# Kernel tuning notes

Measured on AMD Instinct MI355X. Metric: run time of the kernel, lower is better.

## Reference

```python
import jax, jax.numpy as jnp
import numpy as np

ITER_STEPS = 2  # matches init_kwargs iteration_steps


def setup_inputs() -> dict:
    key = jax.random.key(0)
    ks = jax.random.split(key, 7)
    B, N, D = 16, 1024, 128
    s = 1.0 / np.sqrt(D).astype(np.float32)
    return {
        "node": jax.random.normal(ks[0], (B, N, D), jnp.float32),
        "node_mask": jax.random.randint(ks[1], (B, N), 0, 2, jnp.int32),
        "graph": jax.random.randint(ks[2], (B, N, N), 0, 2, jnp.int32),
        "w_weight": jax.random.normal(ks[3], (D, 1), jnp.float32) * s,
        "b_weight": jnp.zeros((1,), jnp.float32),
        "w_self": jax.random.normal(ks[4], (D, D), jnp.float32) * s,
        "b_self": jnp.zeros((D,), jnp.float32),
        "w_left": jax.random.normal(ks[5], (D, D), jnp.float32) * s,
        "w_right": jax.random.normal(ks[6], (D, D), jnp.float32) * s,
    }


def reference(node, node_mask, graph, w_weight, b_weight, w_self, b_self, w_left, w_right):
    B, N, D = node.shape
    dt = node.dtype
    nm = node_mask.astype(dt)
    g = graph.astype(dt)  # graph[:, :N, :N] slice is identity here
    diag = jnp.eye(N, dtype=dt)
    # pairwise validity mask, zero diagonal (no self loops)
    pair = nm[:, None, :] * nm[:, :, None] * (1.0 - diag)
    gl = pair * g            # edges present in graph
    gr = pair * (1.0 - g)    # complement edges
    nnum = gl.sum(-1) + gr.sum(-1)
    # replace_masked_values(nnum, nnum>=1, 1): avoid div-by-zero for isolated nodes
    nnum = jnp.where(nnum >= 1.0, nnum, jnp.ones((), dt))
    ws = []
    for _ in range(ITER_STEPS):
        node_weight = jax.nn.sigmoid(node @ w_weight + b_weight)[..., 0]  # [B, N]
        ws.append(node_weight)
        self_info = node @ w_self + b_self
        # replace_masked_values(weight_bcast, mask, 0) == weight * mask (mask is 0/1)
        left = jnp.einsum('bij,bjd->bid', node_weight[:, None, :] * gl, node @ w_left)
        right = jnp.einsum('bij,bjd->bid', node_weight[:, None, :] * gr, node @ w_right)
        node = jax.nn.relu(self_info + (left + right) / nnum[..., None])
    all_node_weight = jnp.stack(ws, axis=1)  # [B, ITER_STEPS, N]
    return node, all_node_weight
```

## Files before the change

### kernel.cpp

```cpp
#include <hip/hip_runtime.h>
#include <math.h>


constexpr int B = 16, N = 1024, D = 128, ITERS = 2;

typedef unsigned short u16;
typedef unsigned char u8;
typedef unsigned int u32;
typedef __attribute__((ext_vector_type(8))) short short8v;
typedef __attribute__((ext_vector_type(4))) unsigned int uint4v;
typedef __attribute__((ext_vector_type(4))) float float4v;

__device__ inline u16 f32_to_bf16(float f) {
  u32 bits = __float_as_uint(f);
  bits += 0x7FFFu + ((bits >> 16) & 1u);
  return (u16)(bits >> 16);
}

__device__ __forceinline__ short8v expand_byte(u32 by) {
  u32 e0 = ((by & 1u) ? 0x3F80u : 0u) | ((by & 2u) ? 0x3F800000u : 0u);
  u32 e1 = ((by & 4u) ? 0x3F80u : 0u) | ((by & 8u) ? 0x3F800000u : 0u);
  u32 e2 = ((by & 16u) ? 0x3F80u : 0u) | ((by & 32u) ? 0x3F800000u : 0u);
  u32 e3 = ((by & 64u) ? 0x3F80u : 0u) | ((by & 128u) ? 0x3F800000u : 0u);
  uint4v ev = {e0, e1, e2, e3};
  return __builtin_bit_cast(short8v, ev);
}

__device__ __forceinline__ void map_brt(int blk, int& b, int& rt) {
  int slot = blk >> 3;
  b = ((slot >> 6) << 3) | (blk & 7);
  rt = slot & 63;
}

__global__ __launch_bounds__(256) void wpack_kernel(
    const float* __restrict__ w_self, const float* __restrict__ w_left,
    const float* __restrict__ w_right, const int* __restrict__ mask,
    u16* __restrict__ wsF, u16* __restrict__ wlF, u16* __restrict__ wrF,
    float* __restrict__ sb) {
  int blk = blockIdx.x, tid = threadIdx.x;
  if (blk < 12) {
    int widx = blk >> 2, seg = blk & 3;
    const float* W = (widx == 0) ? w_self : (widx == 1) ? w_left : w_right;
    u16* WF = (widx == 0) ? wsF : (widx == 1) ? wlF : wrF;
#pragma unroll
    for (int q = 0; q < 16; ++q) {
      int o = seg * 4096 + q * 256 + tid;
      int e = o & 7, lane = (o >> 3) & 63, ks = (o >> 9) & 3, cblk = o >> 11;
      int c = cblk * 16 + (lane & 15);
      int k = ks * 32 + ((lane >> 4) & 3) * 8 + e;
      WF[o] = f32_to_bf16(W[k * 128 + c]);
    }
  } else {
    int b = tid >> 4, seg = tid & 15;
    const int* mp = mask + b * N + seg * 64;
    int s = 0;
    for (int q = 0; q < 64; ++q) s += mp[q];
    float fs = (float)s;
    fs += __shfl_xor(fs, 8, 16);
    fs += __shfl_xor(fs, 4, 16);
    fs += __shfl_xor(fs, 2, 16);
    fs += __shfl_xor(fs, 1, 16);
    if (seg == 0) sb[b] = fs;
  }
}

__device__ __forceinline__ void prep_body(
    float (*nlds)[132], float* wmrow, float* invrow, int b, int rt, int tid,
    const int* __restrict__ mask, const float* __restrict__ w_weight,
    const float* __restrict__ b_weight, const float* __restrict__ b_self,
    const u16* __restrict__ wsF, const u16* __restrict__ wlF,
    const u16* __restrict__ wrF, const float* __restrict__ sb,
    float* __restrict__ outw_t, float* __restrict__ nsadj, u16* __restrict__ xF,
    float* __restrict__ part) {
  int r0 = rt * 16;
  if (tid < 128) {
    int r = tid >> 3, jj = tid & 7;
    float acc = 0.f;
#pragma unroll
    for (int q = 0; q < 4; ++q) {
      float4 wv = *(const float4*)(w_weight + jj * 16 + q * 4);
      const float* np = &nlds[r][jj * 16 + q * 4];
      acc += np[0] * wv.x + np[1] * wv.y + np[2] * wv.z + np[3] * wv.w;
    }
    acc += __shfl_xor(acc, 4, 8);
    acc += __shfl_xor(acc, 2, 8);
    acc += __shfl_xor(acc, 1, 8);
    if (jj == 0) {
      float w = 1.f / (1.f + expf(-(acc + b_weight[0])));
      outw_t[b * (ITERS * N) + r0 + r] = w;
      float nm = (float)mask[b * N + r0 + r];
      float nnum = fmaxf(nm * (sb[b] - nm), 1.f);
      wmrow[r] = w * nm;
      invrow[r] = nm / nnum;
    }
  }
  __syncthreads();

  int w = tid >> 6, lane = tid & 63;
  int l15 = lane & 15, lg = lane >> 4;
  int ch = w * 32;

  short8v af[4];
#pragma unroll
  for (int ks = 0; ks < 4; ++ks) {
    float tmp[8];
    *(float4*)&tmp[0] = *(const float4*)&nlds[l15][ks * 32 + lg * 8];
    *(float4*)&tmp[4] = *(const float4*)&nlds[l15][ks * 32 + lg * 8 + 4];
    short8v t;
#pragma unroll
    for (int e = 0; e < 8; ++e) t[e] = (short)f32_to_bf16(tmp[e]);
    af[ks] = t;
  }

  float4v aNR[2], aNL[2], aNS[2];
#define RUN_GEMM(WF, ACC)                                                          \
  {                                                                                \
    _Pragma("unroll") for (int cf = 0; cf < 2; ++cf) {                             \
      ACC[cf] = (float4v){0.f, 0.f, 0.f, 0.f};                                     \
      int cblk = w * 2 + cf;                                                       \
      const u16* bp = (WF) + (((cblk * 4) * 64 + lane) << 3);                      \
      _Pragma("unroll") for (int ks = 0; ks < 4; ++ks) {                           \
        short8v bf = *(const short8v*)(bp + ks * 512);                             \
        ACC[cf] =                                                                  \
            __builtin_amdgcn_mfma_f32_16x16x32_bf16(af[ks], bf, ACC[cf], 0, 0, 0); \
      }                                                                            \
    }                                                                              \
  }
  RUN_GEMM(wrF, aNR);
  RUN_GEMM(wlF, aNL);
  RUN_GEMM(wsF, aNS);
#undef RUN_GEMM

  float wmv[4], invv[4];
#pragma unroll
  for (int j = 0; j < 4; ++j) {
    int rloc = lg * 4 + j;
    wmv[j] = wmrow[rloc];
    invv[j] = invrow[rloc];
  }
  int kch = rt >> 1;
  int lane_f = ((rt & 1) * 2 + (lg >> 1)) * 16;
  int e0 = (lg & 1) * 4;
  float pv[2] = {0.f, 0.f};
#pragma unroll
  for (int cf = 0; cf < 2; ++cf) {
    int col = ch + cf * 16 + l15;
    float bsv = b_self[col];
    u16 xb[4];
#pragma unroll
    for (int j = 0; j < 4; ++j) {
      float x = wmv[j] * (aNL[cf][j] - aNR[cf][j]);
      float v = wmv[j] * aNR[cf][j];
      pv[cf] += v;
      nsadj[((size_t)b * N + r0 + lg * 4 + j) * D + col] =
          aNS[cf][j] + bsv - invv[j] * v;
      xb[j] = f32_to_bf16(x);
    }
    int cblk = w * 2 + cf;
    size_t fi = ((((size_t)b * 8 + cblk) * 32 + kch) * 64 + lane_f + l15) * 8 + e0;
    *(ushort4*)&xF[fi] = *(ushort4*)&xb[0];
  }
#pragma unroll
  for (int cf = 0; cf < 2; ++cf) {
    pv[cf] += __shfl_xor(pv[cf], 16);
    pv[cf] += __shfl_xor(pv[cf], 32);
  }
  if (lg == 0) {
#pragma unroll
    for (int cf = 0; cf < 2; ++cf)
      part[((size_t)b * 64 + rt) * 128 + ch + cf * 16 + l15] = pv[cf];
  }
}

__device__ __forceinline__ void agg32_core(
    const u8* __restrict__ gpk, const u16* __restrict__ xF,
    const float* __restrict__ part, const float* __restrict__ sb,
    const int* __restrict__ mask, const float* __restrict__ nsadj, int b, int r0,
    int tid, float (*red)[128], float ov[8]) {
  {
    int col = tid & 127, grp = tid >> 7;
    float s = 0.f;
#pragma unroll
    for (int p = 0; p < 16; ++p)
      s += part[((size_t)b * 64 + grp * 16 + p) * 128 + col];
    red[grp][col] = s;
  }
  int wv = tid >> 6, lane = tid & 63;
  int l15 = lane & 15, lg = lane >> 4;

  const u8* g0 = gpk + ((size_t)b * N + r0 + l15) * 128 + lg * 32;
  uint4 qA = *(const uint4*)g0;
  uint4 qB = *(const uint4*)(g0 + 16);
  uint4 qC = *(const uint4*)(g0 + 16 * 128);
  uint4 qD = *(const uint4*)(g0 + 16 * 128 + 16);
  u32 q0[8] = {qA.x, qA.y, qA.z, qA.w, qB.x, qB.y, qB.z, qB.w};
  u32 q1[8] = {qC.x, qC.y, qC.z, qC.w, qD.x, qD.y, qD.z, qD.w};

  const u16* xb = xF + (((size_t)b * 8 + wv) * 32) * 512 + lane * 8;

  float4v acc0 = {0.f, 0.f, 0.f, 0.f};
  float4v acc1 = {0.f, 0.f, 0.f, 0.f};
  short8v b0 = *(const short8v*)(xb);
  short8v b1 = *(const short8v*)(xb + 512);
#pragma unroll
  for (int cl = 0; cl < 32; ++cl) {
    short8v b2 = b0;
    if (cl + 2 < 32) b2 = *(const short8v*)(xb + (cl + 2) * 512);
    u32 by0 = (q0[cl >> 2] >> ((cl & 3) * 8)) & 255u;
    u32 by1 = (q1[cl >> 2] >> ((cl & 3) * 8)) & 255u;
    short8v a0 = expand_byte(by0);
    short8v a1 = expand_byte(by1);
    acc0 = __builtin_amdgcn_mfma_f32_16x16x32_bf16(a0, b0, acc0, 0, 0, 0);
    acc1 = __builtin_amdgcn_mfma_f32_16x16x32_bf16(a1, b0, acc1, 0, 0, 0);
    b0 = b1;
    b1 = b2;
  }
  __syncthreads();

  float sbv = sb[b];
  int col = wv * 16 + l15;
  float vt = red[0][col] + red[1][col] + red[2][col] + red[3][col];
#pragma unroll
  for (int rs = 0; rs < 2; ++rs) {
#pragma unroll
    for (int j = 0; j < 4; ++j) {
      float a = (rs == 0) ? acc0[j] : acc1[j];
      int orow = r0 + rs * 16 + lg * 4 + j;
      float nm = (float)mask[b * N + orow];
      float nnum = fmaxf(nm * (sbv - nm), 1.f);
      float inv = nm / nnum;
      size_t off = ((size_t)b * N + orow) * D + col;
      ov[rs * 4 + j] = fmaxf(nsadj[off] + inv * (a + vt), 0.f);
    }
  }
}

__device__ __forceinline__ void map_brt32(int blk, int& b, int& rt32) {
  int slot = blk >> 3;
  b = ((slot >> 5) << 3) | (blk & 7);
  rt32 = slot & 31;
}

__global__ __launch_bounds__(256, 4) void pack_prep_kernel(
    const float* __restrict__ node, const int* __restrict__ graph,
    const int* __restrict__ mask, const float* __restrict__ w_weight,
    const float* __restrict__ b_weight, const float* __restrict__ b_self,
    const u16* __restrict__ wsF, const u16* __restrict__ wlF,
    const u16* __restrict__ wrF, const float* __restrict__ sb,
    u8* __restrict__ gpk, float* __restrict__ outw, float* __restrict__ nsadjA,
    u16* __restrict__ xFA, float* __restrict__ partA) {
  __shared__ float nlds[16][132];
  __shared__ float wmrow[16], invrow[16];
  int tid = threadIdx.x;
  int blk = blockIdx.x;

  if (blk < 2048) {
    int gidx0 = blk * 256 + tid;
    int4 ra[4][2];
#pragma unroll
    for (int it = 0; it < 4; ++it) {
      int gidx = gidx0 + it * (2048 * 256);
      int j = gidx & 127, rowg = gidx >> 7;
      const int* gp = graph + ((size_t)rowg << 10) + j * 8;
      ra[it][0] = *(const int4*)gp;
      ra[it][1] = *(const int4*)(gp + 4);
    }
#pragma unroll
    for (int it = 0; it < 4; ++it) {
      int gidx = gidx0 + it * (2048 * 256);
      int j = gidx & 127, rowg = gidx >> 7;
      int i = rowg & (N - 1);
      int4 a = ra[it][0], c = ra[it][1];
      u32 by = (u32)(a.x != 0) | ((u32)(a.y != 0) << 1) | ((u32)(a.z != 0) << 2) |
               ((u32)(a.w != 0) << 3) | ((u32)(c.x != 0) << 4) |
               ((u32)(c.y != 0) << 5) | ((u32)(c.z != 0) << 6) |
               ((u32)(c.w != 0) << 7);
      if (j == (i >> 3)) by &= ~(1u << (i & 7));
      gpk[((size_t)rowg << 7) + (j & 3) * 32 + (j >> 2)] = (u8)by;
    }
    return;
  }

  int pblk = blk - 2048;
  int b, rt;
  map_brt(pblk, b, rt);
  int r0 = rt * 16;

  const float* nbase = node + ((size_t)b * N + r0) * D;
#pragma unroll
  for (int p = 0; p < 2; ++p) {
    int g = p * 256 + tid;
    int row = g >> 5, c4 = g & 31;
    *(float4*)&nlds[row][c4 * 4] = *(const float4*)(nbase + row * 128 + c4 * 4);
  }
  __syncthreads();

  prep_body(nlds, wmrow, invrow, b, rt, tid, mask, w_weight, b_weight, b_self, wsF,
            wlF, wrF, sb, outw, nsadjA, xFA, partA);
}

__global__ __launch_bounds__(512, 4) void agg_prep_kernel(
    const u8* __restrict__ gpk, const int* __restrict__ mask,
    const float* __restrict__ w_weight, const float* __restrict__ b_weight,
    const float* __restrict__ b_self, const u16* __restrict__ wsF,
    const u16* __restrict__ wlF, const u16* __restrict__ wrF,
    const float* __restrict__ sb, const float* __restrict__ nsadjA,
    const u16* __restrict__ xFA, const float* __restrict__ partA,
    float* __restrict__ outw, float* __restrict__ nsadjB, u16* __restrict__ xFB,
    float* __restrict__ partB) {
  __shared__ float red[4][128];
  __shared__ float nlds[32][132];
  __shared__ float wmrow[32], invrow[32];
  int tid = threadIdx.x;
  int b, rt32;
  map_brt32(blockIdx.x, b, rt32);
  int r0 = rt32 * 32;

  float ov[8];
  agg32_core(gpk, xFA, partA, sb, mask, nsadjA, b, r0, tid, red, ov);

  int wv = tid >> 6, lane = tid & 63;
  int l15 = lane & 15, lg = lane >> 4;
  int col = wv * 16 + l15;
#pragma unroll
  for (int rs = 0; rs < 2; ++rs)
#pragma unroll
    for (int j = 0; j < 4; ++j) nlds[rs * 16 + lg * 4 + j][col] = ov[rs * 4 + j];
  __syncthreads();

  int half = tid >> 8;
  int tid2 = tid & 255;
  prep_body((float(*)[132]) & nlds[half * 16][0], &wmrow[half * 16],
            &invrow[half * 16], b, rt32 * 2 + half, tid2, mask, w_weight,
            b_weight, b_self, wsF, wlF, wrF, sb, outw + N, nsadjB, xFB, partB);
}

__global__ __launch_bounds__(512, 4) void agg_fin_kernel(
    const u8* __restrict__ gpk, const int* __restrict__ mask,
    const float* __restrict__ sb, const float* __restrict__ nsadjB,
    const u16* __restrict__ xFB, const float* __restrict__ partB,
    float* __restrict__ out) {
  __shared__ float red[4][128];
  int tid = threadIdx.x;
  int b, rt32;
  map_brt32(blockIdx.x, b, rt32);
  int r0 = rt32 * 32;

  float ov[8];
  agg32_core(gpk, xFB, partB, sb, mask, nsadjB, b, r0, tid, red, ov);

  int wv = tid >> 6, lane = tid & 63;
  int l15 = lane & 15, lg = lane >> 4;
  int col = wv * 16 + l15;
#pragma unroll
  for (int rs = 0; rs < 2; ++rs)
#pragma unroll
    for (int j = 0; j < 4; ++j) {
      int orow = r0 + rs * 16 + lg * 4 + j;
      out[((size_t)b * N + orow) * D + col] = ov[rs * 4 + j];
    }
}

extern "C" void kernel_launch(void* const* d_in, const int* in_sizes, int n_in,
                              void* d_out, int out_size, void* d_ws, size_t ws_size,
                              hipStream_t stream) {
  const float* node0 = (const float*)d_in[0];
  const int* mask = (const int*)d_in[1];
  const int* graph = (const int*)d_in[2];
  const float* w_weight = (const float*)d_in[3];
  const float* b_weight = (const float*)d_in[4];
  const float* w_self = (const float*)d_in[5];
  const float* b_self = (const float*)d_in[6];
  const float* w_left = (const float*)d_in[7];
  const float* w_right = (const float*)d_in[8];
  float* out = (float*)d_out;
  float* outw = out + (size_t)B * N * D;

  char* ws = (char*)d_ws;
  const size_t MB = 1024 * 1024;
  float* nsadjA = (float*)ws;
  float* nsadjB = (float*)(ws + 8 * MB);
  u16* xFA = (u16*)(ws + 16 * MB);
  u16* xFB = (u16*)(ws + 20 * MB);
  u8* gpk = (u8*)(ws + 24 * MB);
  u16* wsF = (u16*)(ws + 26 * MB);
  u16* wlF = wsF + 16384;
  u16* wrF = wlF + 16384;
  float* partA = (float*)(ws + 26 * MB + 3 * 32768);
  float* partB = partA + (size_t)B * 64 * 128;
  float* sb = partB + (size_t)B * 64 * 128;

  wpack_kernel<<<13, 256, 0, stream>>>(w_self, w_left, w_right, mask, wsF, wlF,
                                       wrF, sb);
  pack_prep_kernel<<<3072, 256, 0, stream>>>(node0, graph, mask, w_weight,
                                             b_weight, b_self, wsF, wlF, wrF, sb,
                                             gpk, outw, nsadjA, xFA, partA);
  agg_prep_kernel<<<512, 512, 0, stream>>>(gpk, mask, w_weight, b_weight, b_self,
                                           wsF, wlF, wrF, sb, nsadjA, xFA, partA,
                                           outw, nsadjB, xFB, partB);
  agg_fin_kernel<<<512, 512, 0, stream>>>(gpk, mask, sb, nsadjB, xFB, partB, out);
}
```

Before: 60.66 us.

## Fold weight packing into pack_prep kernel with an atomic grid barrier

The separate weight-pack and mask-sum kernel is removed. Its work now runs in the first 13 blocks of pack_prep_kernel, which publish completion through an atomic counter. The prep blocks spin on that counter before using the packed weights, so one kernel launch and its inter-kernel gap go away. This adds a hipMemsetAsync to reset the counter, and it relies on the producer blocks being scheduled before the spinning blocks. If they are not, the spin could stall until its iteration cap is reached.

```diff
diff --git a/kernel.cpp b/kernel.cpp
--- a/kernel.cpp
+++ b/kernel.cpp
@@ -32,35 +32,17 @@
   rt = slot & 63;
 }
 
-__global__ __launch_bounds__(256) void wpack_kernel(
-    const float* __restrict__ w_self, const float* __restrict__ w_left,
-    const float* __restrict__ w_right, const int* __restrict__ mask,
-    u16* __restrict__ wsF, u16* __restrict__ wlF, u16* __restrict__ wrF,
-    float* __restrict__ sb) {
-  int blk = blockIdx.x, tid = threadIdx.x;
-  if (blk < 12) {
-    int widx = blk >> 2, seg = blk & 3;
-    const float* W = (widx == 0) ? w_self : (widx == 1) ? w_left : w_right;
-    u16* WF = (widx == 0) ? wsF : (widx == 1) ? wlF : wrF;
-#pragma unroll
-    for (int q = 0; q < 16; ++q) {
-      int o = seg * 4096 + q * 256 + tid;
-      int e = o & 7, lane = (o >> 3) & 63, ks = (o >> 9) & 3, cblk = o >> 11;
-      int c = cblk * 16 + (lane & 15);
-      int k = ks * 32 + ((lane >> 4) & 3) * 8 + e;
-      WF[o] = f32_to_bf16(W[k * 128 + c]);
-    }
-  } else {
-    int b = tid >> 4, seg = tid & 15;
-    const int* mp = mask + b * N + seg * 64;
-    int s = 0;
-    for (int q = 0; q < 64; ++q) s += mp[q];
-    float fs = (float)s;
-    fs += __shfl_xor(fs, 8, 16);
-    fs += __shfl_xor(fs, 4, 16);
-    fs += __shfl_xor(fs, 2, 16);
-    fs += __shfl_xor(fs, 1, 16);
-    if (seg == 0) sb[b] = fs;
+__device__ __forceinline__ void map_brt32(int blk, int& b, int& rt32) {
+  int slot = blk >> 3;
+  b = ((slot >> 5) << 3) | (blk & 7);
+  rt32 = slot & 31;
+}
+
+__device__ __forceinline__ void spin_ge(u32* p, u32 v) {
+  int t = 0;
+  while (__hip_atomic_load(p, __ATOMIC_ACQUIRE, __HIP_MEMORY_SCOPE_AGENT) < v) {
+    __builtin_amdgcn_s_sleep(1);
+    if (++t > (1 << 22)) break;
   }
 }
 
@@ -235,26 +217,52 @@
   }
 }
 
-__device__ __forceinline__ void map_brt32(int blk, int& b, int& rt32) {
-  int slot = blk >> 3;
-  b = ((slot >> 5) << 3) | (blk & 7);
-  rt32 = slot & 31;
-}
-
 __global__ __launch_bounds__(256, 4) void pack_prep_kernel(
     const float* __restrict__ node, const int* __restrict__ graph,
     const int* __restrict__ mask, const float* __restrict__ w_weight,
     const float* __restrict__ b_weight, const float* __restrict__ b_self,
-    const u16* __restrict__ wsF, const u16* __restrict__ wlF,
-    const u16* __restrict__ wrF, const float* __restrict__ sb,
+    const float* __restrict__ w_self, const float* __restrict__ w_left,
+    const float* __restrict__ w_right, u16* __restrict__ wsF,
+    u16* __restrict__ wlF, u16* __restrict__ wrF, float* __restrict__ sb,
     u8* __restrict__ gpk, float* __restrict__ outw, float* __restrict__ nsadjA,
-    u16* __restrict__ xFA, float* __restrict__ partA) {
+    u16* __restrict__ xFA, float* __restrict__ partA, u32* bar) {
   __shared__ float nlds[16][132];
   __shared__ float wmrow[16], invrow[16];
   int tid = threadIdx.x;
   int blk = blockIdx.x;
 
   if (blk < 2048) {
+    if (blk < 13) {
+      if (blk < 12) {
+        int widx = blk >> 2, seg = blk & 3;
+        const float* W = (widx == 0) ? w_self : (widx == 1) ? w_left : w_right;
+        u16* WF = (widx == 0) ? wsF : (widx == 1) ? wlF : wrF;
+#pragma unroll
+        for (int q = 0; q < 16; ++q) {
+          int o = seg * 4096 + q * 256 + tid;
+          int e = o & 7, lane = (o >> 3) & 63, ks = (o >> 9) & 3, cblk = o >> 11;
+          int c = cblk * 16 + (lane & 15);
+          int k = ks * 32 + ((lane >> 4) & 3) * 8 + e;
+          WF[o] = f32_to_bf16(W[k * 128 + c]);
+        }
+      } else {
+        int bb = tid >> 4, seg = tid & 15;
+        const int* mp = mask + bb * N + seg * 64;
+        int s = 0;
+        for (int q = 0; q < 64; ++q) s += mp[q];
+        float fs = (float)s;
+        fs += __shfl_xor(fs, 8, 16);
+        fs += __shfl_xor(fs, 4, 16);
+        fs += __shfl_xor(fs, 2, 16);
+        fs += __shfl_xor(fs, 1, 16);
+        if (seg == 0) sb[bb] = fs;
+      }
+      __threadfence();
+      __syncthreads();
+      if (tid == 0)
+        __hip_atomic_fetch_add(&bar[0], 1u, __ATOMIC_ACQ_REL,
+                               __HIP_MEMORY_SCOPE_AGENT);
+    }
     int gidx0 = blk * 256 + tid;
     int4 ra[4][2];
 #pragma unroll
@@ -293,6 +301,7 @@
     int row = g >> 5, c4 = g & 31;
     *(float4*)&nlds[row][c4 * 4] = *(const float4*)(nbase + row * 128 + c4 * 4);
   }
+  if (tid == 0) spin_ge(&bar[0], 13);
   __syncthreads();
 
   prep_body(nlds, wmrow, invrow, b, rt, tid, mask, w_weight, b_weight, b_self, wsF,
@@ -389,12 +398,12 @@
   float* partA = (float*)(ws + 26 * MB + 3 * 32768);
   float* partB = partA + (size_t)B * 64 * 128;
   float* sb = partB + (size_t)B * 64 * 128;
-
-  wpack_kernel<<<13, 256, 0, stream>>>(w_self, w_left, w_right, mask, wsF, wlF,
-                                       wrF, sb);
-  pack_prep_kernel<<<3072, 256, 0, stream>>>(node0, graph, mask, w_weight,
-                                             b_weight, b_self, wsF, wlF, wrF, sb,
-                                             gpk, outw, nsadjA, xFA, partA);
+  u32* bar = (u32*)(ws + 28 * MB);
+
+  hipMemsetAsync(bar, 0, 64, stream);
+  pack_prep_kernel<<<3072, 256, 0, stream>>>(
+      node0, graph, mask, w_weight, b_weight, b_self, w_self, w_left, w_right,
+      wsF, wlF, wrF, sb, gpk, outw, nsadjA, xFA, partA, bar);
   agg_prep_kernel<<<512, 512, 0, stream>>>(gpk, mask, w_weight, b_weight, b_self,
                                            wsF, wlF, wrF, sb, nsadjA, xFA, partA,
                                            outw, nsadjB, xFB, partB);
```

Result: slower. 76.15 us (+25.5%).
